# Kernel optimization log

Measured on AMD Instinct MI355X. Metric: run time of the kernel, lower is better.

The kernel has to match this reference:

```python
import jax, jax.numpy as jnp
import numpy as np

FLOAT_MIN = -100000.0

def setup_inputs() -> dict:
    key = jax.random.key(0)
    ks = jax.random.split(key, 6)
    B, S, Q, K = 16, 8192, 1024, 256
    stdv = 1.0 / np.sqrt(K)
    return {
        "query": jax.random.normal(ks[0], (B, Q), dtype=jnp.float32),
        "keys": jax.random.normal(ks[1], (B, S, K), dtype=jnp.float32),
        "values": jax.random.normal(ks[2], (B, S, K), dtype=jnp.float32),
        "kv_mask": jnp.ones((B, S, 1), dtype=jnp.float32),
        "W_attr": jax.random.uniform(ks[3], (K, Q), jnp.float32, -stdv, stdv),
        "b_attr": jax.random.uniform(ks[4], (K,), jnp.float32, -stdv, stdv),
        "V_attr": jax.random.uniform(ks[5], (K,), jnp.float32, -stdv, stdv),
    }

def reference(query, keys, values, kv_mask, W_attr, b_attr, V_attr):
    # projected query: [B, 1, K]
    q = jnp.einsum('bq,kq->bk', query, W_attr)[:, None, :]
    # additive energies: [B, S, 1]
    energies = jnp.einsum('bsk,k->bs', jnp.tanh(keys + q + b_attr), V_attr)[:, :, None]
    energies = kv_mask * energies + (1.0 - kv_mask) * FLOAT_MIN
    scores = jax.nn.softmax(energies, axis=1)          # [B, S, 1]
    ctx = jnp.sum(values * scores, axis=1)             # [B, V_dim]
    return (scores, ctx)
```

## Files before the change

### kernel.cpp

```cpp
#include <hip/hip_runtime.h>
#include <math.h>

#define BB 16
#define SS 8192
#define KK 256
#define QQ 1024

static constexpr float C2L2E = 2.88539008177792681f;
static constexpr float L2E = 1.44269504088896341f;
static constexpr float FLOAT_MIN_V = -100000.0f;

typedef float floatx4 __attribute__((ext_vector_type(4)));

__device__ __forceinline__ float wave_sum(float v) {
#pragma unroll
  for (int off = 32; off >= 1; off >>= 1) v += __shfl_xor(v, off, 64);
  return v;
}

__device__ __forceinline__ floatx4 ldnt(const float* p) {
  return __builtin_nontemporal_load((const floatx4*)p);
}

__global__ __launch_bounds__(256) void qproj_kernel(
    const float* __restrict__ query, const float* __restrict__ W,
    const float* __restrict__ b_attr, float* __restrict__ qb2) {
  const int blk = blockIdx.x;
  const int b = blk >> 6;
  const int kg = blk & 63;
  const int lane = threadIdx.x & 63;
  const int w = threadIdx.x >> 6;
  const int k = kg * 4 + w;

  const float4* q4 = (const float4*)(query + (size_t)b * QQ);
  const float4* w4 = (const float4*)(W + (size_t)k * QQ);
  float acc = 0.f;
#pragma unroll
  for (int j = 0; j < 4; ++j) {
    const float4 qv = q4[j * 64 + lane];
    const float4 wv = w4[j * 64 + lane];
    acc = fmaf(wv.x, qv.x, acc);
    acc = fmaf(wv.y, qv.y, acc);
    acc = fmaf(wv.z, qv.z, acc);
    acc = fmaf(wv.w, qv.w, acc);
  }
  acc = wave_sum(acc);
  if (lane == 0) qb2[b * KK + k] = C2L2E * (acc + b_attr[k]);
}

#define FROWS 64
__global__ __launch_bounds__(256) void fused_kernel(
    const float* __restrict__ keys, const float* __restrict__ values,
    const float* __restrict__ mask, const float* __restrict__ V_attr,
    const float* __restrict__ qb2, float* __restrict__ pbuf,
    float* __restrict__ part_l, float* __restrict__ part_acc) {
  const int blk = blockIdx.x;
  const int b = blk / (SS / FROWS);
  const int lane = threadIdx.x & 63;
  const int w = threadIdx.x >> 6;
  const int s0 = (blk % (SS / FROWS)) * FROWS + w * (FROWS / 4);

  const float4 v4 = ((const float4*)V_attr)[lane];
  const float sv = wave_sum(v4.x + v4.y + v4.z + v4.w);
  const float4 nv2 =
      make_float4(-2.f * v4.x, -2.f * v4.y, -2.f * v4.z, -2.f * v4.w);
  const float4 qb = ((const float4*)qb2)[b * (KK / 4) + lane];

  const float* krow = keys + (size_t)(b * SS + s0) * KK;
  const float* vrow = values + (size_t)(b * SS + s0) * KK;
  floatx4 kf0 = ldnt(krow + 4 * lane);
  floatx4 vf0 = ldnt(vrow + 4 * lane);
  floatx4 kf1 = ldnt(krow + KK + 4 * lane);
  floatx4 vf1 = ldnt(vrow + KK + 4 * lane);

  float l0 = 0.f, l1 = 0.f;
  float4 acc0 = make_float4(0.f, 0.f, 0.f, 0.f);
  float4 acc1 = make_float4(0.f, 0.f, 0.f, 0.f);
  for (int i = 0; i < FROWS / 4; i += 2) {
    const floatx4 ck0 = kf0, cv0 = vf0, ck1 = kf1, cv1 = vf1;
    if (i + 2 < FROWS / 4) {
      kf0 = ldnt(krow + (size_t)(i + 2) * KK + 4 * lane);
      vf0 = ldnt(vrow + (size_t)(i + 2) * KK + 4 * lane);
      kf1 = ldnt(krow + (size_t)(i + 3) * KK + 4 * lane);
      vf1 = ldnt(vrow + (size_t)(i + 3) * KK + 4 * lane);
    }
    const float mk0 = mask[b * SS + s0 + i];
    const float mk1 = mask[b * SS + s0 + i + 1];

    float p0, p1;
    {
      float a0 = __builtin_amdgcn_rcpf(
          1.f + __builtin_amdgcn_exp2f(fmaf(ck0.x, C2L2E, qb.x)));
      float a1 = __builtin_amdgcn_rcpf(
          1.f + __builtin_amdgcn_exp2f(fmaf(ck0.y, C2L2E, qb.y)));
      float a2 = __builtin_amdgcn_rcpf(
          1.f + __builtin_amdgcn_exp2f(fmaf(ck0.z, C2L2E, qb.z)));
      float a3 = __builtin_amdgcn_rcpf(
          1.f + __builtin_amdgcn_exp2f(fmaf(ck0.w, C2L2E, qb.w)));
      p0 = fmaf(nv2.x, a0, fmaf(nv2.y, a1, fmaf(nv2.z, a2, nv2.w * a3)));
    }
    {
      float a0 = __builtin_amdgcn_rcpf(
          1.f + __builtin_amdgcn_exp2f(fmaf(ck1.x, C2L2E, qb.x)));
      float a1 = __builtin_amdgcn_rcpf(
          1.f + __builtin_amdgcn_exp2f(fmaf(ck1.y, C2L2E, qb.y)));
      float a2 = __builtin_amdgcn_rcpf(
          1.f + __builtin_amdgcn_exp2f(fmaf(ck1.z, C2L2E, qb.z)));
      float a3 = __builtin_amdgcn_rcpf(
          1.f + __builtin_amdgcn_exp2f(fmaf(ck1.w, C2L2E, qb.w)));
      p1 = fmaf(nv2.x, a0, fmaf(nv2.y, a1, fmaf(nv2.z, a2, nv2.w * a3)));
    }
#pragma unroll
    for (int off = 32; off >= 1; off >>= 1) {
      p0 += __shfl_xor(p0, off, 64);
      p1 += __shfl_xor(p1, off, 64);
    }
    const float x0 = mk0 * (p0 + sv) + (1.f - mk0) * FLOAT_MIN_V;
    const float x1 = mk1 * (p1 + sv) + (1.f - mk1) * FLOAT_MIN_V;
    const float pe0 = __builtin_amdgcn_exp2f(x0 * L2E);
    const float pe1 = __builtin_amdgcn_exp2f(x1 * L2E);
    if (lane == 0) {
      pbuf[b * SS + s0 + i] = pe0;
      pbuf[b * SS + s0 + i + 1] = pe1;
    }
    l0 += pe0;
    l1 += pe1;
    acc0.x = fmaf(pe0, cv0.x, acc0.x);
    acc0.y = fmaf(pe0, cv0.y, acc0.y);
    acc0.z = fmaf(pe0, cv0.z, acc0.z);
    acc0.w = fmaf(pe0, cv0.w, acc0.w);
    acc1.x = fmaf(pe1, cv1.x, acc1.x);
    acc1.y = fmaf(pe1, cv1.y, acc1.y);
    acc1.z = fmaf(pe1, cv1.z, acc1.z);
    acc1.w = fmaf(pe1, cv1.w, acc1.w);
  }
  const float l = l0 + l1;
  const float4 acc = make_float4(acc0.x + acc1.x, acc0.y + acc1.y,
                                 acc0.z + acc1.z, acc0.w + acc1.w);

  __shared__ float lacc[4][KK];
  __shared__ float ll[4];
  ((float4*)&lacc[w][0])[lane] = acc;
  if (lane == 0) ll[w] = l;
  __syncthreads();
  const int t = threadIdx.x;
  part_acc[(size_t)blk * KK + t] =
      lacc[0][t] + lacc[1][t] + lacc[2][t] + lacc[3][t];
  if (t == 0) part_l[blk] = ll[0] + ll[1] + ll[2] + ll[3];
}

__global__ __launch_bounds__(1024) void finalize_kernel(
    const float* __restrict__ part_l, const float* __restrict__ part_acc,
    const float* __restrict__ pbuf, float* __restrict__ scores,
    float* __restrict__ ctx) {
  const int b = blockIdx.x;
  const int tid = threadIdx.x;
  const int lane = tid & 63;
  constexpr int NP = SS / FROWS;
  __shared__ float sl[NP];
  __shared__ float cred[4][KK];

  if (tid < NP) sl[tid] = part_l[b * NP + tid];
  __syncthreads();

  const float L = wave_sum(sl[lane] + sl[lane + 64]);
  const float invL = 1.f / L;

  const int g = tid >> 8;
  const int k = tid & 255;
  float s = 0.f;
#pragma unroll 8
  for (int j = g * 32; j < g * 32 + 32; ++j)
    s += part_acc[(size_t)(b * NP + j) * KK + k];
  cred[g][k] = s;
  __syncthreads();
  if (tid < KK)
    ctx[b * KK + tid] =
        (cred[0][tid] + cred[1][tid] + cred[2][tid] + cred[3][tid]) * invL;

#pragma unroll
  for (int i = 0; i < 8; ++i) {
    const int s_idx = tid + i * 1024;
    scores[b * SS + s_idx] = pbuf[b * SS + s_idx] * invL;
  }
}

extern "C" void kernel_launch(void* const* d_in, const int* in_sizes, int n_in,
                              void* d_out, int out_size, void* d_ws,
                              size_t ws_size, hipStream_t stream) {
  const float* query = (const float*)d_in[0];
  const float* keys = (const float*)d_in[1];
  const float* values = (const float*)d_in[2];
  const float* mask = (const float*)d_in[3];
  const float* W = (const float*)d_in[4];
  const float* b_attr = (const float*)d_in[5];
  const float* V_attr = (const float*)d_in[6];

  float* scores = (float*)d_out;
  float* ctx = scores + BB * SS;

  float* qb2 = (float*)d_ws;
  float* pbuf = qb2 + BB * KK;
  float* part_l = pbuf + BB * SS;
  float* part_acc = part_l + BB * (SS / FROWS);

  qproj_kernel<<<BB * (KK / 4), 256, 0, stream>>>(query, W, b_attr, qb2);
  fused_kernel<<<BB * (SS / FROWS), 256, 0, stream>>>(
      keys, values, mask, V_attr, qb2, pbuf, part_l, part_acc);
  finalize_kernel<<<BB, 1024, 0, stream>>>(part_l, part_acc, pbuf, scores,
                                           ctx);
}
```

Measured before the change: 273.2 us.

## Fuse finalize into main kernel via last-block-done atomic counter per batch

Removes the separate finalize kernel launch. Each block increments a per-batch atomic counter after writing its partials, and the last block for that batch reduces the partial sums, writes ctx and normalizes scores. The counters are reset inside the qproj kernel. This saves one launch and the serial tail of a 16-block finalize, at the cost of fences and atomics plus a tail handled by the last block of each batch.

Result: slower. 641.0 us (+134.7%).

```diff
diff --git a/kernel.cpp b/kernel.cpp
--- a/kernel.cpp
+++ b/kernel.cpp
@@ -22,9 +22,17 @@
   return __builtin_nontemporal_load((const floatx4*)p);
 }
 
+#define FROWS 64
+#define NPB (SS / FROWS)
+#define CNT_STRIDE 32
+
 __global__ __launch_bounds__(256) void qproj_kernel(
     const float* __restrict__ query, const float* __restrict__ W,
-    const float* __restrict__ b_attr, float* __restrict__ qb2) {
+    const float* __restrict__ b_attr, float* __restrict__ qb2,
+    unsigned int* __restrict__ cnt) {
+  if (blockIdx.x == 0 && threadIdx.x < BB)
+    cnt[threadIdx.x * CNT_STRIDE] = 0u;
+
   const int blk = blockIdx.x;
   const int b = blk >> 6;
   const int kg = blk & 63;
@@ -48,17 +56,22 @@
   if (lane == 0) qb2[b * KK + k] = C2L2E * (acc + b_attr[k]);
 }
 
-#define FROWS 64
 __global__ __launch_bounds__(256) void fused_kernel(
     const float* __restrict__ keys, const float* __restrict__ values,
     const float* __restrict__ mask, const float* __restrict__ V_attr,
     const float* __restrict__ qb2, float* __restrict__ pbuf,
-    float* __restrict__ part_l, float* __restrict__ part_acc) {
+    float* __restrict__ part_l, float* __restrict__ part_acc,
+    unsigned int* __restrict__ cnt, float* __restrict__ scores,
+    float* __restrict__ ctx) {
   const int blk = blockIdx.x;
-  const int b = blk / (SS / FROWS);
+  const int b = blk / NPB;
   const int lane = threadIdx.x & 63;
   const int w = threadIdx.x >> 6;
-  const int s0 = (blk % (SS / FROWS)) * FROWS + w * (FROWS / 4);
+  const int s0 = (blk % NPB) * FROWS + w * (FROWS / 4);
+
+  __shared__ float lacc[4][KK];
+  __shared__ float ll[4];
+  __shared__ unsigned int sdone;
 
   const float4 v4 = ((const float4*)V_attr)[lane];
   const float sv = wave_sum(v4.x + v4.y + v4.z + v4.w);
@@ -138,8 +151,6 @@
   const float4 acc = make_float4(acc0.x + acc1.x, acc0.y + acc1.y,
                                  acc0.z + acc1.z, acc0.w + acc1.w);
 
-  __shared__ float lacc[4][KK];
-  __shared__ float ll[4];
   ((float4*)&lacc[w][0])[lane] = acc;
   if (lane == 0) ll[w] = l;
   __syncthreads();
@@ -147,41 +158,46 @@
   part_acc[(size_t)blk * KK + t] =
       lacc[0][t] + lacc[1][t] + lacc[2][t] + lacc[3][t];
   if (t == 0) part_l[blk] = ll[0] + ll[1] + ll[2] + ll[3];
-}
-
-__global__ __launch_bounds__(1024) void finalize_kernel(
-    const float* __restrict__ part_l, const float* __restrict__ part_acc,
-    const float* __restrict__ pbuf, float* __restrict__ scores,
-    float* __restrict__ ctx) {
-  const int b = blockIdx.x;
-  const int tid = threadIdx.x;
-  const int lane = tid & 63;
-  constexpr int NP = SS / FROWS;
-  __shared__ float sl[NP];
-  __shared__ float cred[4][KK];
-
-  if (tid < NP) sl[tid] = part_l[b * NP + tid];
-  __syncthreads();
-
-  const float L = wave_sum(sl[lane] + sl[lane + 64]);
+
+  __syncthreads();
+  __threadfence();
+  if (t == 0) sdone = atomicAdd(&cnt[b * CNT_STRIDE], 1u);
+  __syncthreads();
+  if (sdone != NPB - 1) return;
+  __threadfence();
+
+  const float L =
+      wave_sum(part_l[b * NPB + lane] + part_l[b * NPB + 64 + lane]);
   const float invL = 1.f / L;
 
-  const int g = tid >> 8;
-  const int k = tid & 255;
-  float s = 0.f;
+  {
+    const int rg = t >> 6;
+    const float4* pa4 = (const float4*)(part_acc + (size_t)b * NPB * KK);
+    float4 s4 = make_float4(0.f, 0.f, 0.f, 0.f);
 #pragma unroll 8
-  for (int j = g * 32; j < g * 32 + 32; ++j)
-    s += part_acc[(size_t)(b * NP + j) * KK + k];
-  cred[g][k] = s;
-  __syncthreads();
-  if (tid < KK)
-    ctx[b * KK + tid] =
-        (cred[0][tid] + cred[1][tid] + cred[2][tid] + cred[3][tid]) * invL;
-
+    for (int j = rg * 32; j < rg * 32 + 32; ++j) {
+      const float4 v = pa4[(size_t)j * (KK / 4) + lane];
+      s4.x += v.x;
+      s4.y += v.y;
+      s4.z += v.z;
+      s4.w += v.w;
+    }
+    ((float4*)&lacc[rg][0])[lane] = s4;
+  }
+  __syncthreads();
+  ctx[b * KK + t] =
+      (lacc[0][t] + lacc[1][t] + lacc[2][t] + lacc[3][t]) * invL;
+
+  const float4* pb4 = (const float4*)(pbuf + (size_t)b * SS);
+  float4* sc4 = (float4*)(scores + (size_t)b * SS);
 #pragma unroll
   for (int i = 0; i < 8; ++i) {
-    const int s_idx = tid + i * 1024;
-    scores[b * SS + s_idx] = pbuf[b * SS + s_idx] * invL;
+    float4 v = pb4[t + i * 256];
+    v.x *= invL;
+    v.y *= invL;
+    v.z *= invL;
+    v.w *= invL;
+    sc4[t + i * 256] = v;
   }
 }
 
@@ -202,11 +218,12 @@
   float* qb2 = (float*)d_ws;
   float* pbuf = qb2 + BB * KK;
   float* part_l = pbuf + BB * SS;
-  float* part_acc = part_l + BB * (SS / FROWS);
-
-  qproj_kernel<<<BB * (KK / 4), 256, 0, stream>>>(query, W, b_attr, qb2);
-  fused_kernel<<<BB * (SS / FROWS), 256, 0, stream>>>(
-      keys, values, mask, V_attr, qb2, pbuf, part_l, part_acc);
-  finalize_kernel<<<BB, 1024, 0, stream>>>(part_l, part_acc, pbuf, scores,
-                                           ctx);
-}
+  float* part_acc = part_l + BB * NPB;
+  unsigned int* cnt =
+      (unsigned int*)(part_acc + (size_t)BB * NPB * KK);
+
+  qproj_kernel<<<BB * (KK / 4), 256, 0, stream>>>(query, W, b_attr, qb2, cnt);
+  fused_kernel<<<BB * NPB, 256, 0, stream>>>(keys, values, mask, V_attr, qb2,
+                                             pbuf, part_l, part_acc, cnt,
+                                             scores, ctx);
+}
```
